# Performance work log

Measured on AMD Instinct MI355X. Metric: run time of the kernel, lower is better.

## Reference

```python
import jax, jax.numpy as jnp
import numpy as np
from jax import lax

DILATIONS = [1, 2, 4]
L, H, D_IN = 3, 256, 256
T, B = 512, 128


def _lstm_scan(gx, whh, bhh, h0, c0):
    """gx: (Td, N, 4H) precomputed input gates; scan torch LSTMCell recurrence."""
    def step(carry, g_x):
        h, c = carry
        gates = g_x + h @ whh.T + bhh          # (N, 4H), gate order i,f,g,o
        i, f, g, o = jnp.split(gates, 4, axis=-1)
        c = jax.nn.sigmoid(f) * c + jax.nn.sigmoid(i) * jnp.tanh(g)
        h = jax.nn.sigmoid(o) * jnp.tanh(c)
        return (h, c), h
    (_, _), hs = lax.scan(step, (h0, c0), gx)
    return hs                                   # (Td, N, H)


def _dilated_layer(x, wih, whh, b_ih, b_hh, rate):
    """x: (T, B, D). Pack `rate` consecutive steps along batch, run cell, unpack."""
    t, b, d = x.shape
    td = -(-t // rate)                          # ceil division
    pad = td * rate - t
    if pad:
        x = jnp.pad(x, ((0, pad), (0, 0), (0, 0)))
    h = wih.shape[0] // 4
    # torch.cat([x[i*r+j] for j in range(r)], dim=0) == reshape (td, r*b, d)
    xd = x.reshape(td, rate * b, d)
    gx = xd @ wih.T + b_ih                      # hoist input projection out of scan
    h0 = jnp.zeros((rate * b, h), x.dtype)
    hs = _lstm_scan(gx, whh, b_hh, h0, jnp.zeros_like(h0))
    # torch.chunk(out, r, 0) unroll == reshape back to (td*r, b, h), trim pad
    return hs.reshape(td * rate, b, h)[:t]


def setup_inputs() -> dict:
    key = jax.random.key(0)
    ks = jax.random.split(key, 5)
    s = 1.0 / np.sqrt(H)                        # torch LSTMCell init scale
    return {
        "x":   jax.random.normal(ks[0], (T, B, D_IN), jnp.float32),
        "Wih": jax.random.uniform(ks[1], (L, 4 * H, D_IN), jnp.float32, -s, s),
        "Whh": jax.random.uniform(ks[2], (L, 4 * H, H), jnp.float32, -s, s),
        "bih": jax.random.uniform(ks[3], (L, 4 * H), jnp.float32, -s, s),
        "bhh": jax.random.uniform(ks[4], (L, 4 * H), jnp.float32, -s, s),
    }


def reference(x, Wih, Whh, bih, bhh):
    outs = []
    cur = x
    for l, rate in enumerate(DILATIONS):
        cur = _dilated_layer(cur, Wih[l], Whh[l], bih[l], bhh[l], rate)
        outs.append(cur)
    return jnp.stack(outs, axis=0)              # (L, T, B, H)
```

## Files before the change

### kernel.cpp

```cpp
#include <hip/hip_runtime.h>


typedef _Float16 half8   __attribute__((ext_vector_type(8)));
typedef _Float16 half4_t __attribute__((ext_vector_type(4)));
typedef float    floatx4 __attribute__((ext_vector_type(4)));

__device__ __forceinline__ float sigmf(float x) {
    return 1.0f / (1.0f + __expf(-x));
}
__device__ __forceinline__ float tanhfast(float x) {
    float e = __expf(-2.0f * fabsf(x));
    float r = (1.0f - e) / (1.0f + e);
    return copysignf(r, x);
}

#define MFMA16(A, B, C) __builtin_amdgcn_mfma_f32_16x16x32_f16((A), (B), (C), 0, 0, 0)

typedef __attribute__((address_space(3))) unsigned int lds_u32;
typedef __attribute__((address_space(1))) unsigned int glb_u32;

__device__ __forceinline__ void gload_lds16(const _Float16* g, _Float16* l) {
    __builtin_amdgcn_global_load_lds((const glb_u32*)g, (lds_u32*)l, 16, 0, 0);
}

__global__ void prep_kernel(
    const float* __restrict__ Wih, const float* __restrict__ Whh,
    const float* __restrict__ bih, const float* __restrict__ bhh,
    _Float16* __restrict__ wihp, _Float16* __restrict__ whhp,
    float* __restrict__ biasc)
{
    int id = blockIdx.x * 256 + threadIdx.x;
    if (id < 196608) {
        int u = id;
        const float* W = Whh; _Float16* P = whhp;
        if (u >= 98304) { W = Wih; P = wihp; u -= 98304; }
        int ln = u & 63; u >>= 6;
        int ks = u & 7;  u >>= 3;
        int ct = u & 7;  u >>= 3;
        int w  = u & 7;  u >>= 3;
        int l  = u;
        int col = (ct >> 1) * 256 + w * 32 + (ct & 1) * 16 + (ln & 15);
        int k0  = ks * 32 + (ln >> 4) * 8;
        const float* src = W + ((size_t)l * 1024 + col) * 256 + k0;
        half8 hv;
#pragma unroll
        for (int j = 0; j < 8; ++j) hv[j] = (_Float16)src[j];
        *(half8*)(P + (size_t)l * 262144 +
                  (size_t)(((w * 8 + ct) * 8 + ks) * 64 + ln) * 8) = hv;
    } else if (id < 199680) {
        int v = id - 196608;
        biasc[v] = bih[v] + bhh[v];
    }
}

template<int F16IN>
__global__ __launch_bounds__(512, 2) void gx_kernel(
    const float* __restrict__ in32,
    const _Float16* __restrict__ in16,
    const _Float16* __restrict__ wpack,
    const float* __restrict__ biasc,
    _Float16* __restrict__ gx,
    int rate, int SG, int S)
{
    __shared__ _Float16 Ab[64][264];
    const int tid = threadIdx.x, lane = tid & 63, w = tid >> 6;
    const int t = blockIdx.x / SG, sg = blockIdx.x % SG;
    const int r15 = lane & 15, q = lane >> 4;

#pragma unroll
    for (int i = 0; i < 4; ++i) {
        int id = tid + 512 * i;
        int row = id >> 5, c16 = id & 31;
        int n = sg * 64 + row;
        size_t base = ((size_t)(t * rate + (n >> 7)) * 128 + (n & 127)) * 256 + c16 * 8;
        if (F16IN) {
            *(uint4*)&Ab[row][c16 * 8] = *(const uint4*)(in16 + base);
        } else {
            floatx4 v0 = *(const floatx4*)(in32 + base);
            floatx4 v1 = *(const floatx4*)(in32 + base + 4);
            half8 hv;
            hv[0] = (_Float16)v0[0]; hv[1] = (_Float16)v0[1];
            hv[2] = (_Float16)v0[2]; hv[3] = (_Float16)v0[3];
            hv[4] = (_Float16)v1[0]; hv[5] = (_Float16)v1[1];
            hv[6] = (_Float16)v1[2]; hv[7] = (_Float16)v1[3];
            *(half8*)&Ab[row][c16 * 8] = hv;
        }
    }
    __syncthreads();

    floatx4 zero4 = {0.f, 0.f, 0.f, 0.f};
    floatx4 acc[4][8];
#pragma unroll
    for (int rt = 0; rt < 4; ++rt)
#pragma unroll
        for (int ct = 0; ct < 8; ++ct) acc[rt][ct] = zero4;

    const _Float16* wsp = wpack + (size_t)w * 32768 + (size_t)lane * 8;
    half8 bfA[8], bfB[8];
#pragma unroll
    for (int ct = 0; ct < 8; ++ct)
        bfA[ct] = *(const half8*)(wsp + (ct * 8 + 0) * 512);

#define AKS(ks, bufC, bufN) { \
    if ((ks) + 1 < 8) { _Pragma("unroll") \
        for (int ct = 0; ct < 8; ++ct) \
            bufN[ct] = *(const half8*)(wsp + (ct * 8 + ((ks) + 1)) * 512); } \
    half8 a0 = *(const half8*)&Ab[ 0 + r15][(ks) * 32 + q * 8]; \
    half8 a1 = *(const half8*)&Ab[16 + r15][(ks) * 32 + q * 8]; \
    half8 a2 = *(const half8*)&Ab[32 + r15][(ks) * 32 + q * 8]; \
    half8 a3 = *(const half8*)&Ab[48 + r15][(ks) * 32 + q * 8]; \
    _Pragma("unroll") for (int ct = 0; ct < 8; ++ct) { \
        acc[0][ct] = MFMA16(a0, bufC[ct], acc[0][ct]); \
        acc[1][ct] = MFMA16(a1, bufC[ct], acc[1][ct]); \
        acc[2][ct] = MFMA16(a2, bufC[ct], acc[2][ct]); \
        acc[3][ct] = MFMA16(a3, bufC[ct], acc[3][ct]); } }

    AKS(0, bfA, bfB); AKS(1, bfB, bfA); AKS(2, bfA, bfB); AKS(3, bfB, bfA);
    AKS(4, bfA, bfB); AKS(5, bfB, bfA); AKS(6, bfA, bfB); AKS(7, bfB, bfA);
#undef AKS

    float be[4], bo_[4];
#pragma unroll
    for (int cp = 0; cp < 4; ++cp) {
        be[cp]  = biasc[cp * 256 + w * 32 + r15];
        bo_[cp] = biasc[cp * 256 + w * 32 + 16 + r15];
    }
#pragma unroll
    for (int rt = 0; rt < 4; ++rt) {
        int sb = sg * 4 + rt;
#pragma unroll
        for (int cp = 0; cp < 4; ++cp) {
            half8 hv;
#pragma unroll
            for (int rg = 0; rg < 4; ++rg) {
                hv[rg]     = (_Float16)(acc[rt][2 * cp][rg]     + be[cp]);
                hv[4 + rg] = (_Float16)(acc[rt][2 * cp + 1][rg] + bo_[cp]);
            }
            *(half8*)(gx + ((((size_t)t * S + sb) * 8 + w) * 4 + cp) * 512 +
                      (size_t)lane * 8) = hv;
        }
    }
}

#define ISSUE(buf, ks) { \
    buf[0] = *(const half8*)(wspi + (3 * 8 + (ks)) * 512); \
    buf[1] = *(const half8*)(wspi + (4 * 8 + (ks)) * 512); \
    buf[2] = *(const half8*)(wspi + (5 * 8 + (ks)) * 512); \
    buf[3] = *(const half8*)(wspi + (6 * 8 + (ks)) * 512); \
    buf[4] = *(const half8*)(wspi + (7 * 8 + (ks)) * 512); }

#define DOKS(ks, buf) { \
    acc[0] = MFMA16(af[ks], rw[0][ks], acc[0]); \
    acc[1] = MFMA16(af[ks], rw[1][ks], acc[1]); \
    acc[2] = MFMA16(af[ks], rw[2][ks], acc[2]); \
    acc[3] = MFMA16(af[ks], buf[0], acc[3]); \
    acc[4] = MFMA16(af[ks], buf[1], acc[4]); \
    acc[5] = MFMA16(af[ks], buf[2], acc[5]); \
    acc[6] = MFMA16(af[ks], buf[3], acc[6]); \
    acc[7] = MFMA16(af[ks], buf[4], acc[7]); }

__global__ __launch_bounds__(512, 2) void scan_kernel(
    const _Float16* __restrict__ gx,
    const _Float16* __restrict__ wpack,
    float* __restrict__ out,
    _Float16* __restrict__ h16,
    int rate, int td, int S)
{
    __shared__ _Float16 Hb[2][16][264];
    __shared__ _Float16 Gx[8][4][64][8];

    const int tid  = threadIdx.x;
    const int lane = tid & 63;
    const int w    = tid >> 6;
    const int sb   = blockIdx.x;
    const int r15  = lane & 15;
    const int q    = lane >> 4;

    const _Float16* wsp = wpack + (size_t)w * 32768 + (size_t)lane * 8;

    half8 rw[3][8];
#pragma unroll
    for (int ct = 0; ct < 3; ++ct)
#pragma unroll
        for (int ks = 0; ks < 8; ++ks)
            rw[ct][ks] = *(const half8*)(wsp + (ct * 8 + ks) * 512);

    for (int i = tid; i < 2 * 16 * 264; i += 512)
        (&Hb[0][0][0])[i] = (_Float16)0.0f;

    {
        const _Float16* g0 = gx + (((size_t)0 * S + sb) * 8 + (size_t)w) * 2048;
#pragma unroll
        for (int cp = 0; cp < 4; ++cp)
            gload_lds16(g0 + cp * 512 + (size_t)lane * 8, &Gx[w][cp][0][0]);
    }
    __syncthreads();

    float cst[8], hprev[8];
#pragma unroll
    for (int i = 0; i < 8; ++i) { cst[i] = 0.f; hprev[i] = 0.f; }

    for (int t = 0; t < td; ++t) {
        const int rd = t & 1, wr = rd ^ 1;

        const _Float16* wspi = wsp;
        asm volatile("" : "+v"(wspi));

        half8 sA[5], sB[5];
        ISSUE(sA, 0); ISSUE(sB, 1);

        half8 af[8];
#pragma unroll
        for (int ks = 0; ks < 8; ++ks)
            af[ks] = *(const half8*)&Hb[rd][r15][ks * 32 + q * 8];

        floatx4 acc[8];
#pragma unroll
        for (int cp = 0; cp < 4; ++cp) {
            half8 gv = *(const half8*)&Gx[w][cp][lane][0];
#pragma unroll
            for (int rg = 0; rg < 4; ++rg) {
                acc[2 * cp][rg]     = (float)gv[rg];
                acc[2 * cp + 1][rg] = (float)gv[4 + rg];
            }
        }

        DOKS(0, sA); ISSUE(sA, 2);
        DOKS(1, sB); ISSUE(sB, 3);
        DOKS(2, sA); ISSUE(sA, 4);
        DOKS(3, sB); ISSUE(sB, 5);
        DOKS(4, sA); ISSUE(sA, 6);
        DOKS(5, sB); ISSUE(sB, 7);

        {
            int tn = (t + 1 < td) ? (t + 1) : t;
            const _Float16* gn = gx + (((size_t)tn * S + sb) * 8 + (size_t)w) * 2048;
#pragma unroll
            for (int cp = 0; cp < 4; ++cp)
                gload_lds16(gn + cp * 512 + (size_t)lane * 8, &Gx[w][cp][0][0]);
        }

        if (t > 0) {
#pragma unroll
            for (int s = 0; s < 2; ++s)
#pragma unroll
                for (int rg = 0; rg < 4; ++rg) {
                    int row = q * 4 + rg, n = sb * 16 + row;
                    int hid = w * 32 + s * 16 + r15;
                    size_t off = ((size_t)((t - 1) * rate + (n >> 7)) * 128 +
                                  (n & 127)) * 256 + hid;
                    float hv = hprev[s * 4 + rg];
                    out[off] = hv;
                    h16[off] = (_Float16)hv;
                }
        }

        DOKS(6, sA);
        DOKS(7, sB);

#pragma unroll
        for (int s = 0; s < 2; ++s)
#pragma unroll
            for (int rg = 0; rg < 4; ++rg) {
                int ci = s * 4 + rg;
                float gi = acc[0 + s][rg], gf = acc[2 + s][rg];
                float gg = acc[4 + s][rg], go = acc[6 + s][rg];
                float c = sigmf(gf) * cst[ci] + sigmf(gi) * tanhfast(gg);
                cst[ci] = c;
                float hv = sigmf(go) * tanhfast(c);
                hprev[ci] = hv;
                Hb[wr][q * 4 + rg][w * 32 + s * 16 + r15] = (_Float16)hv;
            }

        __syncthreads();
    }

#pragma unroll
    for (int s = 0; s < 2; ++s)
#pragma unroll
        for (int rg = 0; rg < 4; ++rg) {
            int row = q * 4 + rg, n = sb * 16 + row;
            int hid = w * 32 + s * 16 + r15;
            size_t off = ((size_t)((td - 1) * rate + (n >> 7)) * 128 +
                          (n & 127)) * 256 + hid;
            float hv = hprev[s * 4 + rg];
            out[off] = hv;
            h16[off] = (_Float16)hv;
        }
}

#undef ISSUE
#undef DOKS

#define GH 16
#define NB 32
#define RING_SLOTS 4
#define RING_STRIDE (512 * 256)
#define RING_BYTES  (RING_SLOTS * RING_STRIDE * 2)
#define CNT_INTS    6144

__global__ __launch_bounds__(256) void lstm_layer_kernel(
    const float* __restrict__ in,
    const float* __restrict__ Wih,
    const float* __restrict__ Whh,
    const float* __restrict__ bih,
    const float* __restrict__ bhh,
    float* __restrict__ out,
    _Float16* __restrict__ ring,
    int* __restrict__ cnt,
    int rate, int td, int G_b)
{
    __shared__ _Float16 Abuf[NB][520];
    __shared__ float scr[NB][68];

    const int tid  = threadIdx.x;
    const int lane = tid & 63;
    const int wv   = tid >> 6;
    const int g_b  = blockIdx.x % G_b;
    const int g_h  = blockIdx.x / G_b;
    const int hid0 = g_h * 16;
    const int n0   = g_b * NB;

    half8 bfrag[16];
    {
        const int col  = lane & 15;
        const int qq   = lane >> 4;
        const int grow = wv * 256 + hid0 + col;
        const float* wih_row = Wih + (size_t)grow * 256;
        const float* whh_row = Whh + (size_t)grow * 256;
#pragma unroll
        for (int ks = 0; ks < 16; ++ks) {
            const int k0 = ks * 32 + qq * 8;
            const float* src = (k0 < 256) ? (wih_row + k0) : (whh_row + (k0 - 256));
            floatx4 w0 = *(const floatx4*)(src);
            floatx4 w1 = *(const floatx4*)(src + 4);
            half8 hb;
            hb[0] = (_Float16)w0[0]; hb[1] = (_Float16)w0[1];
            hb[2] = (_Float16)w0[2]; hb[3] = (_Float16)w0[3];
            hb[4] = (_Float16)w1[0]; hb[5] = (_Float16)w1[1];
            hb[6] = (_Float16)w1[2]; hb[7] = (_Float16)w1[3];
            bfrag[ks] = hb;
        }
    }

    const int erow = tid >> 4;
    const int ehid = tid & 15;
    const float bi = bih[0 * 256 + hid0 + ehid] + bhh[0 * 256 + hid0 + ehid];
    const float bf = bih[1 * 256 + hid0 + ehid] + bhh[1 * 256 + hid0 + ehid];
    const float bg = bih[2 * 256 + hid0 + ehid] + bhh[2 * 256 + hid0 + ehid];
    const float bo = bih[3 * 256 + hid0 + ehid] + bhh[3 * 256 + hid0 + ehid];
    float c0 = 0.0f, c1 = 0.0f;

    floatx4 xp[8];
#pragma unroll
    for (int i = 0; i < 8; ++i) {
        int id  = tid + 256 * i;
        int row = id >> 6;
        int m   = n0 + row;
        const float* p = in + ((size_t)(0 * rate + (m >> 7)) * 128 + (m & 127)) * 256
                         + (size_t)(id & 63) * 4;
        xp[i] = *(const floatx4*)p;
    }

    for (int t = 0; t < td; ++t) {
#pragma unroll
        for (int i = 0; i < 8; ++i) {
            int id  = tid + 256 * i;
            int row = id >> 6;
            int c4  = (id & 63) * 4;
            half4_t hx;
            hx[0] = (_Float16)xp[i][0]; hx[1] = (_Float16)xp[i][1];
            hx[2] = (_Float16)xp[i][2]; hx[3] = (_Float16)xp[i][3];
            *(half4_t*)&Abuf[row][c4] = hx;
        }
        if (t + 1 < td) {
#pragma unroll
            for (int i = 0; i < 8; ++i) {
                int id  = tid + 256 * i;
                int row = id >> 6;
                int m   = n0 + row;
                const float* p = in + ((size_t)((t + 1) * rate + (m >> 7)) * 128 + (m & 127)) * 256
                                 + (size_t)(id & 63) * 4;
                xp[i] = *(const floatx4*)p;
            }
        }
        if (t > 0) {
            const int ci = g_b * td + (t - 1);
            if (tid == 0) {
                while (__hip_atomic_load(&cnt[ci], __ATOMIC_RELAXED,
                                         __HIP_MEMORY_SCOPE_AGENT) < GH) {
                    __builtin_amdgcn_s_sleep(1);
                }
            }
            __syncthreads();
            (void)__hip_atomic_load(&cnt[ci], __ATOMIC_ACQUIRE, __HIP_MEMORY_SCOPE_AGENT);
            const _Float16* rs = ring + (size_t)((t - 1) & 3) * RING_STRIDE;
#pragma unroll
            for (int i = 0; i < 4; ++i) {
                int id  = tid + 256 * i;
                int row = id >> 5;
                int kc  = id & 31;
                int m   = n0 + row;
                uint4 v = *(const uint4*)(rs + (size_t)m * 256 + kc * 8);
                *(uint4*)&Abuf[row][256 + kc * 8] = v;
            }
        } else {
#pragma unroll
            for (int i = 0; i < 4; ++i) {
                int id  = tid + 256 * i;
                int row = id >> 5;
                int kc  = id & 31;
                uint4 z = {0u, 0u, 0u, 0u};
                *(uint4*)&Abuf[row][256 + kc * 8] = z;
            }
        }
        __syncthreads();

        floatx4 acc0 = {0.f, 0.f, 0.f, 0.f};
        floatx4 acc1 = {0.f, 0.f, 0.f, 0.f};
        {
            const int r  = lane & 15;
            const int qq = lane >> 4;
#pragma unroll
            for (int ks = 0; ks < 16; ++ks) {
                half8 a0 = *(const half8*)&Abuf[r][ks * 32 + qq * 8];
                half8 a1 = *(const half8*)&Abuf[16 + r][ks * 32 + qq * 8];
                acc0 = MFMA16(a0, bfrag[ks], acc0);
                acc1 = MFMA16(a1, bfrag[ks], acc1);
            }
        }
        {
            const int r  = lane & 15;
            const int qq = lane >> 4;
#pragma unroll
            for (int reg = 0; reg < 4; ++reg) {
                scr[qq * 4 + reg][wv * 16 + r]      = acc0[reg];
                scr[16 + qq * 4 + reg][wv * 16 + r] = acc1[reg];
            }
        }
        __syncthreads();

        {
            float gi0 = scr[erow][ehid]           + bi;
            float gf0 = scr[erow][16 + ehid]      + bf;
            float gg0 = scr[erow][32 + ehid]      + bg;
            float go0 = scr[erow][48 + ehid]      + bo;
            float gi1 = scr[16 + erow][ehid]      + bi;
            float gf1 = scr[16 + erow][16 + ehid] + bf;
            float gg1 = scr[16 + erow][32 + ehid] + bg;
            float go1 = scr[16 + erow][48 + ehid] + bo;

            c0 = sigmf(gf0) * c0 + sigmf(gi0) * tanhfast(gg0);
            c1 = sigmf(gf1) * c1 + sigmf(gi1) * tanhfast(gg1);
            float h0v = sigmf(go0) * tanhfast(c0);
            float h1v = sigmf(go1) * tanhfast(c1);

            int m0 = n0 + erow, m1 = m0 + 16;
            int tau0 = t * rate + (m0 >> 7);
            int tau1 = t * rate + (m1 >> 7);
            out[((size_t)tau0 * 128 + (m0 & 127)) * 256 + hid0 + ehid] = h0v;
            out[((size_t)tau1 * 128 + (m1 & 127)) * 256 + hid0 + ehid] = h1v;

            _Float16* rw_ = ring + (size_t)(t & 3) * RING_STRIDE;
            rw_[(size_t)m0 * 256 + hid0 + ehid] = (_Float16)h0v;
            rw_[(size_t)m1 * 256 + hid0 + ehid] = (_Float16)h1v;
        }

        __syncthreads();
        if (tid == 0) {
            __hip_atomic_fetch_add(&cnt[g_b * td + t], 1, __ATOMIC_RELEASE,
                                   __HIP_MEMORY_SCOPE_AGENT);
        }
    }
}

extern "C" void kernel_launch(void* const* d_in, const int* in_sizes, int n_in,
                              void* d_out, int out_size, void* d_ws, size_t ws_size,
                              hipStream_t stream) {
    const float* x   = (const float*)d_in[0];
    const float* Wih = (const float*)d_in[1];
    const float* Whh = (const float*)d_in[2];
    const float* bih = (const float*)d_in[3];
    const float* bhh = (const float*)d_in[4];
    float* out = (float*)d_out;

    const size_t GX_BYTES  = 134217728ull;
    const size_t H16_BYTES = 33554432ull;
    const size_t WP_BYTES  = 1572864ull;
    const size_t NEED = GX_BYTES + H16_BYTES + 2 * WP_BYTES + 12288ull;

    if (ws_size >= NEED) {
        _Float16* gxb  = (_Float16*)d_ws;
        _Float16* h16  = (_Float16*)((char*)d_ws + GX_BYTES);
        _Float16* whhp = (_Float16*)((char*)d_ws + GX_BYTES + H16_BYTES);
        _Float16* wihp = (_Float16*)((char*)d_ws + GX_BYTES + H16_BYTES + WP_BYTES);
        float* biasc   = (float*)((char*)d_ws + GX_BYTES + H16_BYTES + 2 * WP_BYTES);

        prep_kernel<<<dim3(780), dim3(256), 0, stream>>>(
            Wih, Whh, bih, bhh, wihp, whhp, biasc);

        const int rates[3] = {1, 2, 4};
        for (int l = 0; l < 3; ++l) {
            const int rate = rates[l];
            const int td = 512 / rate;
            const int S  = rate * 8;
            const int SG = S / 4;
            float* out_l = out + (size_t)l * 512 * 128 * 256;
            if (l == 0)
                gx_kernel<0><<<dim3(td * SG), dim3(512), 0, stream>>>(
                    x, nullptr, wihp + (size_t)l * 262144, biasc + l * 1024,
                    gxb, rate, SG, S);
            else
                gx_kernel<1><<<dim3(td * SG), dim3(512), 0, stream>>>(
                    nullptr, h16, wihp + (size_t)l * 262144, biasc + l * 1024,
                    gxb, rate, SG, S);
            scan_kernel<<<dim3(S), dim3(512), 0, stream>>>(
                gxb, whhp + (size_t)l * 262144, out_l, h16, rate, td, S);
        }
        return;
    }

    _Float16* ring = (_Float16*)d_ws;
    int* cnt = (int*)((char*)d_ws + RING_BYTES);
    hipMemsetAsync(cnt, 0, CNT_INTS * sizeof(int), stream);

    const int rates[3]  = {1, 2, 4};
    const int cntOff[3] = {0, 2048, 4096};
    const float* in_ptr = x;
    for (int l = 0; l < 3; ++l) {
        const int rate = rates[l];
        const int td   = 512 / rate;
        const int N    = rate * 128;
        const int G_b  = N / NB;
        lstm_layer_kernel<<<dim3(G_b * GH), dim3(256), 0, stream>>>(
            in_ptr,
            Wih + (size_t)l * 1024 * 256,
            Whh + (size_t)l * 1024 * 256,
            bih + (size_t)l * 1024,
            bhh + (size_t)l * 1024,
            out + (size_t)l * 512 * 128 * 256,
            ring, cnt + cntOff[l],
            rate, td, G_b);
        in_ptr = out + (size_t)l * 512 * 128 * 256;
    }
}
```

Measured before the change: 5.410 ms.

## Split scan hidden dimension across block pairs exchanging h via global ring

The recurrent scan now splits each 16-row batch group across two workgroups, each owning half the hidden units. Each holds its 4 gate tiles of Whh in registers instead of streaming most of them every step. The halves swap h through a global fp16 ring buffer, with per-step atomic counters and spin-waits replacing purely local LDS sharing. This doubles the number of scan blocks and cuts per-step MFMA and weight-load work per block, at the cost of a cross-block synchronisation with global-memory latency on every timestep.

```diff
diff --git a/kernel.cpp b/kernel.cpp
--- a/kernel.cpp
+++ b/kernel.cpp
@@ -22,6 +22,12 @@
 __device__ __forceinline__ void gload_lds16(const _Float16* g, _Float16* l) {
     __builtin_amdgcn_global_load_lds((const glb_u32*)g, (lds_u32*)l, 16, 0, 0);
 }
+
+#define RING_SLOTS 4
+#define RING_STRIDE (512 * 256)
+#define RING_BYTES  (RING_SLOTS * RING_STRIDE * 2)
+#define CNT_PER_LAYER 8192
+#define CNT_INTS      24576
 
 __global__ void prep_kernel(
     const float* __restrict__ Wih, const float* __restrict__ Whh,
@@ -54,7 +60,9 @@
 }
 
 template<int F16IN>
-__global__ __launch_bounds__(512, 2) void gx_kernel(
+__global__ __attribute__((amdgpu_flat_work_group_size(512, 512)))
+__attribute__((amdgpu_waves_per_eu(2, 2)))
+void gx_kernel(
     const float* __restrict__ in32,
     const _Float16* __restrict__ in16,
     const _Float16* __restrict__ wpack,
@@ -142,162 +150,173 @@
     }
 }
 
-#define ISSUE(buf, ks) { \
-    buf[0] = *(const half8*)(wspi + (3 * 8 + (ks)) * 512); \
-    buf[1] = *(const half8*)(wspi + (4 * 8 + (ks)) * 512); \
-    buf[2] = *(const half8*)(wspi + (5 * 8 + (ks)) * 512); \
-    buf[3] = *(const half8*)(wspi + (6 * 8 + (ks)) * 512); \
-    buf[4] = *(const half8*)(wspi + (7 * 8 + (ks)) * 512); }
-
-#define DOKS(ks, buf) { \
-    acc[0] = MFMA16(af[ks], rw[0][ks], acc[0]); \
-    acc[1] = MFMA16(af[ks], rw[1][ks], acc[1]); \
-    acc[2] = MFMA16(af[ks], rw[2][ks], acc[2]); \
-    acc[3] = MFMA16(af[ks], buf[0], acc[3]); \
-    acc[4] = MFMA16(af[ks], buf[1], acc[4]); \
-    acc[5] = MFMA16(af[ks], buf[2], acc[5]); \
-    acc[6] = MFMA16(af[ks], buf[3], acc[6]); \
-    acc[7] = MFMA16(af[ks], buf[4], acc[7]); }
-
-__global__ __launch_bounds__(512, 2) void scan_kernel(
+__global__ __attribute__((amdgpu_flat_work_group_size(512, 512)))
+__attribute__((amdgpu_waves_per_eu(2, 2)))
+void scan2_kernel(
     const _Float16* __restrict__ gx,
     const _Float16* __restrict__ wpack,
     float* __restrict__ out,
     _Float16* __restrict__ h16,
-    int rate, int td, int S)
+    _Float16* __restrict__ ring,
+    int* __restrict__ cnt,
+    int rate, int td, int NB8)
 {
-    __shared__ _Float16 Hb[2][16][264];
-    __shared__ _Float16 Gx[8][4][64][8];
+    __shared__ _Float16 own[2][16][136];
+    __shared__ _Float16 Gx[4][4][64][8];
 
     const int tid  = threadIdx.x;
     const int lane = tid & 63;
     const int w    = tid >> 6;
-    const int sb   = blockIdx.x;
     const int r15  = lane & 15;
     const int q    = lane >> 4;
-
-    const _Float16* wsp = wpack + (size_t)w * 32768 + (size_t)lane * 8;
-
-    half8 rw[3][8];
-#pragma unroll
-    for (int ct = 0; ct < 3; ++ct)
-#pragma unroll
-        for (int ks = 0; ks < 8; ++ks)
-            rw[ct][ks] = *(const half8*)(wsp + (ct * 8 + ks) * 512);
-
-    for (int i = tid; i < 2 * 16 * 264; i += 512)
-        (&Hb[0][0][0])[i] = (_Float16)0.0f;
-
+    const int bg   = blockIdx.x % NB8;
+    const int hh   = blockIdx.x / NB8;
+    const int n0   = bg * 16;
+    const int myb  = blockIdx.x;
+    const int sib  = (hh ^ 1) * NB8 + bg;
+    const int hidg = hh * 128 + w * 16 + r15;
+
+    half8 wf[4][8];
     {
-        const _Float16* g0 = gx + (((size_t)0 * S + sb) * 8 + (size_t)w) * 2048;
-#pragma unroll
-        for (int cp = 0; cp < 4; ++cp)
-            gload_lds16(g0 + cp * 512 + (size_t)lane * 8, &Gx[w][cp][0][0]);
-    }
-    __syncthreads();
-
-    float cst[8], hprev[8];
-#pragma unroll
-    for (int i = 0; i < 8; ++i) { cst[i] = 0.f; hprev[i] = 0.f; }
+        const int w8 = hh * 4 + (w >> 1), b = w & 1;
+#pragma unroll
+        for (int g = 0; g < 4; ++g)
+#pragma unroll
+            for (int ks = 0; ks < 8; ++ks)
+                wf[g][ks] = *(const half8*)(wpack +
+                    (size_t)(((w8 * 8 + 2 * g + b) * 8 + ks) * 64 + lane) * 8);
+    }
+
+    for (int i = tid; i < 16 * 136; i += 512)
+        (&own[0][0][0])[i] = (_Float16)0.0f;
+
+#pragma unroll
+    for (int j = 0; j < 2; ++j) {
+        int gi = w * 2 + j, a = gi >> 2, part = gi & 3;
+        const _Float16* src = gx +
+            ((((size_t)0 * NB8 + bg) * 8 + (hh * 4 + a)) * 4 + part) * 512 +
+            (size_t)lane * 8;
+        gload_lds16(src, &Gx[a][part][0][0]);
+    }
+
+    float cst[4] = {0.f, 0.f, 0.f, 0.f};
+    float hv[4];
 
     for (int t = 0; t < td; ++t) {
         const int rd = t & 1, wr = rd ^ 1;
 
-        const _Float16* wspi = wsp;
-        asm volatile("" : "+v"(wspi));
-
-        half8 sA[5], sB[5];
-        ISSUE(sA, 0); ISSUE(sB, 1);
-
         half8 af[8];
-#pragma unroll
-        for (int ks = 0; ks < 8; ++ks)
-            af[ks] = *(const half8*)&Hb[rd][r15][ks * 32 + q * 8];
-
-        floatx4 acc[8];
-#pragma unroll
-        for (int cp = 0; cp < 4; ++cp) {
-            half8 gv = *(const half8*)&Gx[w][cp][lane][0];
-#pragma unroll
-            for (int rg = 0; rg < 4; ++rg) {
-                acc[2 * cp][rg]     = (float)gv[rg];
-                acc[2 * cp + 1][rg] = (float)gv[4 + rg];
-            }
-        }
-
-        DOKS(0, sA); ISSUE(sA, 2);
-        DOKS(1, sB); ISSUE(sB, 3);
-        DOKS(2, sA); ISSUE(sA, 4);
-        DOKS(3, sB); ISSUE(sB, 5);
-        DOKS(4, sA); ISSUE(sA, 6);
-        DOKS(5, sB); ISSUE(sB, 7);
-
-        {
-            int tn = (t + 1 < td) ? (t + 1) : t;
-            const _Float16* gn = gx + (((size_t)tn * S + sb) * 8 + (size_t)w) * 2048;
-#pragma unroll
-            for (int cp = 0; cp < 4; ++cp)
-                gload_lds16(gn + cp * 512 + (size_t)lane * 8, &Gx[w][cp][0][0]);
-        }
-
         if (t > 0) {
-#pragma unroll
-            for (int s = 0; s < 2; ++s)
-#pragma unroll
-                for (int rg = 0; rg < 4; ++rg) {
-                    int row = q * 4 + rg, n = sb * 16 + row;
-                    int hid = w * 32 + s * 16 + r15;
-                    size_t off = ((size_t)((t - 1) * rate + (n >> 7)) * 128 +
-                                  (n & 127)) * 256 + hid;
-                    float hv = hprev[s * 4 + rg];
-                    out[off] = hv;
-                    h16[off] = (_Float16)hv;
+            const int ci = sib * td + (t - 1);
+            if (tid == 0) {
+                while (__hip_atomic_load(&cnt[ci], __ATOMIC_RELAXED,
+                                         __HIP_MEMORY_SCOPE_AGENT) < 1) {
+                    __builtin_amdgcn_s_sleep(1);
                 }
-        }
-
-        DOKS(6, sA);
-        DOKS(7, sB);
-
-#pragma unroll
-        for (int s = 0; s < 2; ++s)
-#pragma unroll
-            for (int rg = 0; rg < 4; ++rg) {
-                int ci = s * 4 + rg;
-                float gi = acc[0 + s][rg], gf = acc[2 + s][rg];
-                float gg = acc[4 + s][rg], go = acc[6 + s][rg];
-                float c = sigmf(gf) * cst[ci] + sigmf(gi) * tanhfast(gg);
-                cst[ci] = c;
-                float hv = sigmf(go) * tanhfast(c);
-                hprev[ci] = hv;
-                Hb[wr][q * 4 + rg][w * 32 + s * 16 + r15] = (_Float16)hv;
-            }
+            }
+            __syncthreads();
+            (void)__hip_atomic_load(&cnt[ci], __ATOMIC_ACQUIRE,
+                                    __HIP_MEMORY_SCOPE_AGENT);
+            const _Float16* rs = ring + (size_t)((t - 1) & 3) * RING_STRIDE +
+                                 (size_t)(n0 + r15) * 256;
+            if (hh == 0) {
+                af[4] = *(const half8*)(rs + 4 * 32 + q * 8);
+                af[5] = *(const half8*)(rs + 5 * 32 + q * 8);
+                af[6] = *(const half8*)(rs + 6 * 32 + q * 8);
+                af[7] = *(const half8*)(rs + 7 * 32 + q * 8);
+            } else {
+                af[0] = *(const half8*)(rs + 0 * 32 + q * 8);
+                af[1] = *(const half8*)(rs + 1 * 32 + q * 8);
+                af[2] = *(const half8*)(rs + 2 * 32 + q * 8);
+                af[3] = *(const half8*)(rs + 3 * 32 + q * 8);
+            }
+        } else {
+            __syncthreads();
+            half8 z;
+#pragma unroll
+            for (int j = 0; j < 8; ++j) z[j] = (_Float16)0.0f;
+            if (hh == 0) { af[4] = z; af[5] = z; af[6] = z; af[7] = z; }
+            else         { af[0] = z; af[1] = z; af[2] = z; af[3] = z; }
+        }
+
+        floatx4 acc[4];
+#pragma unroll
+        for (int g = 0; g < 4; ++g) {
+            half4_t gv = *(const half4_t*)&Gx[w >> 1][g][lane][(w & 1) * 4];
+#pragma unroll
+            for (int rg = 0; rg < 4; ++rg) acc[g][rg] = (float)gv[rg];
+        }
+
+        if (hh == 0) {
+            af[0] = *(const half8*)&own[rd][r15][0 * 32 + q * 8];
+            af[1] = *(const half8*)&own[rd][r15][1 * 32 + q * 8];
+            af[2] = *(const half8*)&own[rd][r15][2 * 32 + q * 8];
+            af[3] = *(const half8*)&own[rd][r15][3 * 32 + q * 8];
+        } else {
+            af[4] = *(const half8*)&own[rd][r15][0 * 32 + q * 8];
+            af[5] = *(const half8*)&own[rd][r15][1 * 32 + q * 8];
+            af[6] = *(const half8*)&own[rd][r15][2 * 32 + q * 8];
+            af[7] = *(const half8*)&own[rd][r15][3 * 32 + q * 8];
+        }
+
+#define DO_KS(ks) { \
+        acc[0] = MFMA16(af[ks], wf[0][ks], acc[0]); \
+        acc[1] = MFMA16(af[ks], wf[1][ks], acc[1]); \
+        acc[2] = MFMA16(af[ks], wf[2][ks], acc[2]); \
+        acc[3] = MFMA16(af[ks], wf[3][ks], acc[3]); }
+        if (hh == 0) {
+            DO_KS(0) DO_KS(1) DO_KS(2) DO_KS(3)
+            DO_KS(4) DO_KS(5) DO_KS(6) DO_KS(7)
+        } else {
+            DO_KS(4) DO_KS(5) DO_KS(6) DO_KS(7)
+            DO_KS(0) DO_KS(1) DO_KS(2) DO_KS(3)
+        }
+#undef DO_KS
+
+        _Float16* rngw = ring + (size_t)(t & 3) * RING_STRIDE;
+#pragma unroll
+        for (int rg = 0; rg < 4; ++rg) {
+            float gi = acc[0][rg], gf = acc[1][rg];
+            float gg = acc[2][rg], go = acc[3][rg];
+            float c = sigmf(gf) * cst[rg] + sigmf(gi) * tanhfast(gg);
+            cst[rg] = c;
+            float h = sigmf(go) * tanhfast(c);
+            hv[rg] = h;
+            own[wr][q * 4 + rg][w * 16 + r15] = (_Float16)h;
+            rngw[(size_t)(n0 + q * 4 + rg) * 256 + hidg] = (_Float16)h;
+        }
 
         __syncthreads();
-    }
-
-#pragma unroll
-    for (int s = 0; s < 2; ++s)
+        if (tid == 0) {
+            __hip_atomic_fetch_add(&cnt[myb * td + t], 1, __ATOMIC_RELEASE,
+                                   __HIP_MEMORY_SCOPE_AGENT);
+        }
+
 #pragma unroll
         for (int rg = 0; rg < 4; ++rg) {
-            int row = q * 4 + rg, n = sb * 16 + row;
-            int hid = w * 32 + s * 16 + r15;
-            size_t off = ((size_t)((td - 1) * rate + (n >> 7)) * 128 +
-                          (n & 127)) * 256 + hid;
-            float hv = hprev[s * 4 + rg];
-            out[off] = hv;
-            h16[off] = (_Float16)hv;
-        }
-}
-
-#undef ISSUE
-#undef DOKS
+            int n = n0 + q * 4 + rg;
+            int tau = t * rate + (n >> 7);
+            size_t off = ((size_t)tau * 128 + (n & 127)) * 256 + hidg;
+            out[off] = hv[rg];
+            h16[off] = (_Float16)hv[rg];
+        }
+
+        if (t + 1 < td) {
+#pragma unroll
+            for (int j = 0; j < 2; ++j) {
+                int gi = w * 2 + j, a = gi >> 2, part = gi & 3;
+                const _Float16* src = gx +
+                    ((((size_t)(t + 1) * NB8 + bg) * 8 + (hh * 4 + a)) * 4 + part) * 512 +
+                    (size_t)lane * 8;
+                gload_lds16(src, &Gx[a][part][0][0]);
+            }
+        }
+    }
+}
 
 #define GH 16
 #define NB 32
-#define RING_SLOTS 4
-#define RING_STRIDE (512 * 256)
-#define RING_BYTES  (RING_SLOTS * RING_STRIDE * 2)
-#define CNT_INTS    6144
+#define FB_CNT_INTS 6144
 
 __global__ __launch_bounds__(256) void lstm_layer_kernel(
     const float* __restrict__ in,
@@ -484,45 +503,52 @@
     const float* bhh = (const float*)d_in[4];
     float* out = (float*)d_out;
 
-    const size_t GX_BYTES  = 134217728ull;
-    const size_t H16_BYTES = 33554432ull;
-    const size_t WP_BYTES  = 1572864ull;
-    const size_t NEED = GX_BYTES + H16_BYTES + 2 * WP_BYTES + 12288ull;
+    const size_t GX_BYTES   = 134217728ull;
+    const size_t H16_BYTES  = 33554432ull;
+    const size_t WP_BYTES   = 1572864ull;
+    const size_t BIAS_BYTES = 12288ull;
+    const size_t NEED = GX_BYTES + H16_BYTES + 2 * WP_BYTES + BIAS_BYTES +
+                        RING_BYTES + CNT_INTS * sizeof(int);
 
     if (ws_size >= NEED) {
-        _Float16* gxb  = (_Float16*)d_ws;
-        _Float16* h16  = (_Float16*)((char*)d_ws + GX_BYTES);
-        _Float16* whhp = (_Float16*)((char*)d_ws + GX_BYTES + H16_BYTES);
-        _Float16* wihp = (_Float16*)((char*)d_ws + GX_BYTES + H16_BYTES + WP_BYTES);
-        float* biasc   = (float*)((char*)d_ws + GX_BYTES + H16_BYTES + 2 * WP_BYTES);
-
+        char* p = (char*)d_ws;
+        _Float16* gxb  = (_Float16*)p;                 p += GX_BYTES;
+        _Float16* h16  = (_Float16*)p;                 p += H16_BYTES;
+        _Float16* whhp = (_Float16*)p;                 p += WP_BYTES;
+        _Float16* wihp = (_Float16*)p;                 p += WP_BYTES;
+        float*    biasc= (float*)p;                    p += BIAS_BYTES;
+        _Float16* ring = (_Float16*)p;                 p += RING_BYTES;
+        int*      cnt  = (int*)p;
+
+        hipMemsetAsync(cnt, 0, CNT_INTS * sizeof(int), stream);
         prep_kernel<<<dim3(780), dim3(256), 0, stream>>>(
             Wih, Whh, bih, bhh, wihp, whhp, biasc);
 
         const int rates[3] = {1, 2, 4};
         for (int l = 0; l < 3; ++l) {
             const int rate = rates[l];
-            const int td = 512 / rate;
-            const int S  = rate * 8;
-            const int SG = S / 4;
+            const int td   = 512 / rate;
+            const int NB8  = rate * 8;
+            const int SG   = NB8 / 4;
             float* out_l = out + (size_t)l * 512 * 128 * 256;
             if (l == 0)
                 gx_kernel<0><<<dim3(td * SG), dim3(512), 0, stream>>>(
                     x, nullptr, wihp + (size_t)l * 262144, biasc + l * 1024,
-                    gxb, rate, SG, S);
+                    gxb, rate, SG, NB8);
             else
                 gx_kernel<1><<<dim3(td * SG), dim3(512), 0, stream>>>(
                     nullptr, h16, wihp + (size_t)l * 262144, biasc + l * 1024,
-                    gxb, rate, SG, S);
-            scan_kernel<<<dim3(S), dim3(512), 0, stream>>>(
-                gxb, whhp + (size_t)l * 262144, out_l, h16, rate, td, S);
+                    gxb, rate, SG, NB8);
+            scan2_kernel<<<dim3(2 * NB8), dim3(512), 0, stream>>>(
+                gxb, whhp + (size_t)l * 262144, out_l, h16, ring,
+                cnt + l * CNT_PER_LAYER, rate, td, NB8);
         }
         return;
     }
 
     _Float16* ring = (_Float16*)d_ws;
     int* cnt = (int*)((char*)d_ws + RING_BYTES);
-    hipMemsetAsync(cnt, 0, CNT_INTS * sizeof(int), stream);
+    hipMemsetAsync(cnt, 0, FB_CNT_INTS * sizeof(int), stream);
 
     const int rates[3]  = {1, 2, 4};
     const int cntOff[3] = {0, 2048, 4096};
```

Result: faster. 5.221 ms (-3.5%).
